# Performance work log

Measured on AMD Instinct MI355X. Metric: run time of the kernel, lower is better.

Reference implementation:

```python
import jax, jax.numpy as jnp
import numpy as np

B, T, N = 8, 512, 64        # batch, seq_len, enc_in
E, H, P = 128, 256, 96      # embed_size, hidden_size, pred_len
LAMBDA = 0.001              # softshrink sparsity threshold
SCALE = 0.02


def _leaky(h):
    return jnp.where(h >= 0, h, 0.01 * h)


def _softshrink(y):
    return jnp.where(y > LAMBDA, y - LAMBDA, jnp.where(y < -LAMBDA, y + LAMBDA, jnp.zeros_like(y)))


def setup_inputs() -> dict:
    key = jax.random.key(0)
    ks = jax.random.split(key, 16)
    f32 = jnp.float32
    d = {
        "x": jax.random.normal(ks[0], (B, T, N), f32),
        "emb": jax.random.normal(ks[1], (1, E), f32),
        # MLP (embed_size -> hidden -> embed_size), stored as [in, out]
        "w1": SCALE * jax.random.normal(ks[2], (E, H), f32),
        "b1": SCALE * jax.random.normal(ks[3], (H,), f32),
        "w2": SCALE * jax.random.normal(ks[4], (H, E), f32),
        "b2": SCALE * jax.random.normal(ks[5], (E,), f32),
        # MLP_time (seq_len -> hidden -> seq_len)
        "tw1": SCALE * jax.random.normal(ks[6], (T, H), f32),
        "tb1": SCALE * jax.random.normal(ks[7], (H,), f32),
        "tw2": SCALE * jax.random.normal(ks[8], (H, T), f32),
        "tb2": SCALE * jax.random.normal(ks[9], (T,), f32),
        # fc (seq_len*embed -> hidden -> pred_len)
        "fw1": SCALE * jax.random.normal(ks[10], (T * E, H), f32),
        "fb1": SCALE * jax.random.normal(ks[11], (H,), f32),
        "fw2": SCALE * jax.random.normal(ks[12], (H, P), f32),
        "fb2": SCALE * jax.random.normal(ks[13], (P,), f32),
    }
    return d


def reference(x, emb, w1, b1, w2, b2, tw1, tb1, tw2, tb2, fw1, fb1, fw2, fb2):
    # x: [B, T, N]
    x_noD = jnp.transpose(x, (0, 2, 1))            # [B, N, T]
    xe = x_noD[..., None] * emb                    # tokenEmb -> [B, N, T, E]
    bias = xe + x_noD[..., None]

    # NorMLP_temporal: rfft over time, shared MLP on real/imag, softshrink, irfft
    xf = jnp.fft.rfft(xe, axis=2, norm="ortho")   # [B, N, T//2+1, E] complex64

    def mlp(z):
        return _leaky(z @ w1 + b1) @ w2 + b2

    yr = _softshrink(mlp(xf.real))
    yi = _softshrink(mlp(xf.imag))
    y = jax.lax.complex(yr, yi)
    xt = jnp.fft.irfft(y, n=T, axis=2, norm="ortho")  # [B, N, T, E]

    # NorMLP_temporal_WO_freq: MLP_time over last (time) dim of x_noD
    xn = _leaky(x_noD @ tw1 + tb1) @ tw2 + tb2        # [B, N, T]

    out = xt + xn[..., None] + bias                   # use_bias = 1

    flat = out.reshape(B, N, T * E)
    h = _leaky(flat @ fw1 + fb1) @ fw2 + fb2          # [B, N, P]
    return jnp.transpose(h, (0, 2, 1))                # [B, P, N]
```

## Files before the change

kernel.cpp:

```cpp
#include <hip/hip_runtime.h>
#include <hip/hip_bf16.h>


typedef unsigned int uint;
typedef unsigned short ushort_t;
typedef __attribute__((ext_vector_type(4))) float f32x4;
typedef __attribute__((ext_vector_type(8))) short short8;

#define LAMBDA_ 0.001f
#define RSQRT512 0.044194173824159220f

__device__ __forceinline__ ushort_t f2bf(float f) {
    uint u = __float_as_uint(f);
    uint r = (u + 0x7FFFu + ((u >> 16) & 1u)) >> 16;
    return (ushort_t)r;
}
__device__ __forceinline__ ushort_t f2bf_hw(float f) {
    union { __hip_bfloat16 h; ushort_t u; } c;
    c.h = __float2bfloat16(f);
    return c.u;
}
__device__ __forceinline__ float bf2f(ushort_t v) { return __uint_as_float(((uint)v) << 16); }
__device__ __forceinline__ float leaky_(float v) { return v >= 0.f ? v : 0.01f * v; }

__device__ __forceinline__ void gload_lds16(const ushort_t* g, ushort_t* l) {
    __builtin_amdgcn_global_load_lds((const __attribute__((address_space(1))) void*)g,
                                     (__attribute__((address_space(3))) void*)l, 16, 0, 0);
}

__global__ __launch_bounds__(256) void k_pre(const float* __restrict__ x, const float* __restrict__ tw1,
                                             const float* __restrict__ tw2,
                                             ushort_t* __restrict__ A1cat, ushort_t* __restrict__ B1cat,
                                             ushort_t* __restrict__ Wt, ushort_t* __restrict__ tw2_bf) {
    __shared__ float tile[64 * 65];
    int bid = blockIdx.x;
    int tid = threadIdx.x;
    if (bid < 3072) {
        int region = bid >> 10;
        int id = ((bid & 1023) << 8) + tid;
        int a = id >> 9, c = id & 511;
        if (region == 0) {
            int f = (a <= 256) ? a : (a - 256);
            int m = (c * f) & 511;
            float ang = (float)m * (6.283185307179586f / 512.0f);
            float v = ((a <= 256) ? cosf(ang) : -sinf(ang)) * RSQRT512;
            ushort_t hi = f2bf(v);
            ushort_t lo = f2bf(v - bf2f(hi));
            size_t row = (size_t)a * 1536;
            B1cat[row + c] = hi;
            B1cat[row + 512 + c] = hi;
            B1cat[row + 1024 + c] = lo;
        } else if (region == 1) {
            int f = (a <= 256) ? a : (a - 256);
            int m = (c * f) & 511;
            float ang = (float)m * (6.283185307179586f / 512.0f);
            float v = ((a <= 256) ? cosf(ang) : -sinf(ang)) * RSQRT512;
            float sc = (a == 0 || a == 256) ? 1.0f : 2.0f;
            Wt[id] = f2bf(v * sc);
        } else {
            if ((bid & 1023) < 512) tw2_bf[id] = f2bf(tw2[id]);
        }
    } else if (bid < 3104) {
        int b = bid - 3072;
        int t0 = (b & 7) << 6, h0 = (b >> 3) << 6;
        float (*t64)[65] = (float(*)[65])tile;
        for (int i = 0; i < 16; ++i) {
            int idx = tid + i * 256;
            int r = idx >> 6, cc = idx & 63;
            t64[r][cc] = tw1[(size_t)(t0 + r) * 256 + h0 + cc];
        }
        __syncthreads();
        for (int i = 0; i < 16; ++i) {
            int idx = tid + i * 256;
            int rr = idx >> 6, cc2 = idx & 63;
            float v = t64[cc2][rr];
            ushort_t hi = f2bf(v);
            ushort_t lo = f2bf(v - bf2f(hi));
            size_t row = (size_t)(512 + h0 + rr) * 1536;
            int t = t0 + cc2;
            B1cat[row + t] = hi;
            B1cat[row + 512 + t] = hi;
            B1cat[row + 1024 + t] = lo;
        }
    } else {
        int b = bid - 3104;
        int bb = b >> 5;
        int rem = b & 31;
        int t0 = (rem >> 1) << 5;
        int n0 = (rem & 1) << 5;
        int tx = tid & 31, ty = tid >> 5;
        float (*t32)[33] = (float(*)[33])tile;
        for (int i = 0; i < 4; ++i) {
            int tt = ty * 4 + i;
            t32[tt][tx] = x[(size_t)(bb * 512 + t0 + tt) * 64 + n0 + tx];
        }
        __syncthreads();
        for (int i = 0; i < 4; ++i) {
            int nn = ty * 4 + i;
            float v = t32[tx][nn];
            ushort_t hi = f2bf(v);
            ushort_t lo = f2bf(v - bf2f(hi));
            size_t row = (size_t)(bb * 64 + n0 + nn) * 1536;
            int t = t0 + tx;
            A1cat[row + t] = hi;
            A1cat[row + 512 + t] = lo;
            A1cat[row + 1024 + t] = hi;
        }
    }
}

__global__ __launch_bounds__(256) void k_prep1(const float* __restrict__ emb, const float* __restrict__ w1,
                                               const float* __restrict__ b1,
                                               float* __restrict__ u_g, int* __restrict__ idxs_g,
                                               float* __restrict__ bpkey_g) {
    __shared__ float key_s[256];
    __shared__ int idx_s[256];
    int tid = threadIdx.x;
    float acc = 0.f;
#pragma unroll 8
    for (int e = 0; e < 128; ++e) acc += emb[e] * w1[e * 256 + tid];
    u_g[tid] = acc;
    float bb0 = b1[tid];
    key_s[tid] = (acc == 0.f) ? INFINITY : (-bb0 / acc);
    idx_s[tid] = tid;
    __syncthreads();
    for (int k = 2; k <= 256; k <<= 1) {
        for (int j = k >> 1; j > 0; j >>= 1) {
            int ixj = tid ^ j;
            if (ixj > tid) {
                bool up = ((tid & k) == 0);
                float a0 = key_s[tid], a1 = key_s[ixj];
                if ((a0 > a1) == up) {
                    key_s[tid] = a1; key_s[ixj] = a0;
                    int t0 = idx_s[tid]; idx_s[tid] = idx_s[ixj]; idx_s[ixj] = t0;
                }
            }
            __syncthreads();
        }
    }
    bpkey_g[tid] = key_s[tid];
    idxs_g[tid] = idx_s[tid];
}

__global__ __launch_bounds__(256) void k_prep2(const float* __restrict__ u_g, const float* __restrict__ b1,
                                               const float* __restrict__ w2, const float* __restrict__ b2,
                                               const int* __restrict__ idxs_g,
                                               ushort_t* __restrict__ Atab, ushort_t* __restrict__ Btab) {
    __shared__ float sA[256], sB[256];
    int e = blockIdx.x, r = threadIdx.x;
    float uu0 = u_g[r], bb0 = b1[r];
    float w0 = w2[r * 128 + e];
    float c = (uu0 < 0.f || (uu0 == 0.f && bb0 >= 0.f)) ? 1.0f : 0.01f;
    float bA = c * uu0 * w0, bB = c * bb0 * w0;
    int h = idxs_g[r];
    float uu = u_g[h], bb = b1[h];
    float w = w2[h * 128 + e];
    float sgn = (uu > 0.f) ? 0.99f : -0.99f;
    float dA = sgn * uu * w, dB = sgn * bb * w;
    sA[r] = bA; sB[r] = bB;
    __syncthreads();
    for (int off = 128; off > 0; off >>= 1) {
        if (r < off) { sA[r] += sA[r + off]; sB[r] += sB[r + off]; }
        __syncthreads();
    }
    float baseA = sA[0], baseB = sB[0] + b2[e];
    __syncthreads();
    sA[r] = dA; sB[r] = dB;
    __syncthreads();
    for (int off = 1; off < 256; off <<= 1) {
        float vA = (r >= off) ? sA[r - off] : 0.f;
        float vB = (r >= off) ? sB[r - off] : 0.f;
        __syncthreads();
        sA[r] += vA; sB[r] += vB;
        __syncthreads();
    }
    if (r == 0) { Atab[e] = f2bf(baseA); Btab[e] = f2bf(baseB); }
    Atab[(r + 1) * 128 + e] = f2bf(baseA + sA[r]);
    Btab[(r + 1) * 128 + e] = f2bf(baseB + sB[r]);
}

__global__ __launch_bounds__(256) void k_transpose_fw1(const float* __restrict__ fw1, ushort_t* __restrict__ fw1T) {
    __shared__ float tile[64][65];
    int bid = blockIdx.x;
    int e  = bid & 127;
    int hb = (bid >> 7) & 3;
    int tt = bid >> 9;
    int t0 = tt << 6, h0 = hb << 6;
    int tid = threadIdx.x;
    for (int i = 0; i < 4; ++i) {
        int idx = tid + i * 256;
        int r = idx >> 4, c4 = idx & 15;
        const float* src = fw1 + ((size_t)(t0 + r) * 128 + e) * 256 + h0 + c4 * 4;
        float4 v = *(const float4*)src;
        tile[r][c4 * 4 + 0] = v.x;
        tile[r][c4 * 4 + 1] = v.y;
        tile[r][c4 * 4 + 2] = v.z;
        tile[r][c4 * 4 + 3] = v.w;
    }
    __syncthreads();
    for (int p = 0; p < 2; ++p) {
        int idx = tid + p * 256;
        int hh = idx >> 3, tg = idx & 7;
        short8 o;
        for (int j = 0; j < 8; ++j) o[j] = (short)f2bf(tile[tg * 8 + j][hh]);
        *(short8*)(fw1T + ((size_t)(h0 + hh) * 128 + e) * 512 + t0 + tg * 8) = o;
    }
}

__global__ __launch_bounds__(256) void k_reduce_F2(const ushort_t* __restrict__ fw1T, const float* __restrict__ emb,
                                                   float* __restrict__ F1T) {
    __shared__ float embs[128];
    int h = blockIdx.x;
    int tid = threadIdx.x;
    if (tid < 128) embs[tid] = 1.f + emb[tid];
    __syncthreads();
    int t2 = tid * 2;
    const ushort_t* base = fw1T + ((size_t)h << 16) + t2;
    float as0 = 0.f, as1 = 0.f, ae0 = 0.f, ae1 = 0.f;
#pragma unroll 4
    for (int e = 0; e < 128; ++e) {
        uint v = *(const uint*)(base + (size_t)e * 512);
        float v0 = bf2f((ushort_t)(v & 0xffff));
        float v1 = bf2f((ushort_t)(v >> 16));
        float w = embs[e];
        as0 += v0; as1 += v1;
        ae0 += w * v0; ae1 += w * v1;
    }
    F1T[(size_t)h * 512 + t2] = as0;
    F1T[(size_t)h * 512 + t2 + 1] = as1;
    F1T[131072 + (size_t)h * 512 + t2] = ae0;
    F1T[131072 + (size_t)h * 512 + t2 + 1] = ae1;
}

__global__ __launch_bounds__(64) void k_pack_F(const float* __restrict__ F1sT, const float* __restrict__ F1eT,
                                               const float* __restrict__ tb2,
                                               ushort_t* __restrict__ B1cat, ushort_t* __restrict__ F1sT_bf,
                                               float* __restrict__ p2v) {
    int h = blockIdx.x;
    int lane = threadIdx.x;
    int t = lane * 8;
    float p2 = 0.f;
    short8 shi, ehi, elo;
    for (int j = 0; j < 8; ++j) {
        float vs = F1sT[(size_t)h * 512 + t + j];
        float ve = F1eT[(size_t)h * 512 + t + j];
        p2 += tb2[t + j] * vs;
        shi[j] = (short)f2bf(vs);
        ushort_t hi = f2bf(ve);
        ehi[j] = (short)hi;
        elo[j] = (short)f2bf(ve - bf2f(hi));
    }
    *(short8*)(F1sT_bf + (size_t)h * 512 + t) = shi;
    size_t row = (size_t)(768 + h) * 1536;
    *(short8*)(B1cat + row + t) = ehi;
    *(short8*)(B1cat + row + 512 + t) = ehi;
    *(short8*)(B1cat + row + 1024 + t) = elo;
    for (int o = 32; o > 0; o >>= 1) p2 += __shfl_xor(p2, o);
    if (lane == 0) p2v[h] = p2;
}

__global__ __launch_bounds__(256) void k_g1(const ushort_t* __restrict__ A, const ushort_t* __restrict__ Bm,
                                            float* __restrict__ partialG) {
    __shared__ ushort_t As[128 * 72];
    __shared__ ushort_t Bs[128 * 72];
    int tid = threadIdx.x;
    int lane = tid & 63, wid = tid >> 6;
    int wr = wid >> 1, wc = wid & 1;
    int bid = blockIdx.x;
    int kch = bid & 7, tilei = bid >> 3;
    int nt = tilei & 7, mt = tilei >> 3;
    int m0 = mt * 128, n0 = nt * 128;
    f32x4 acc[4][4] = {};
    for (int kt = 0; kt < 3; ++kt) {
        int kb = kch * 192 + kt * 64;
        __syncthreads();
        {
            uint4 va[4], vb[4];
            for (int i = 0; i < 4; ++i) {
                int q = tid + i * 256;
                int row = q >> 3, kcc = (q & 7) << 3;
                va[i] = *(const uint4*)(A + (size_t)(m0 + row) * 1536 + kb + kcc);
                vb[i] = *(const uint4*)(Bm + (size_t)(n0 + row) * 1536 + kb + kcc);
            }
            for (int i = 0; i < 4; ++i) {
                int q = tid + i * 256;
                int row = q >> 3, kcc = (q & 7) << 3;
                *(uint4*)&As[row * 72 + kcc] = va[i];
                *(uint4*)&Bs[row * 72 + kcc] = vb[i];
            }
        }
        __syncthreads();
        for (int ks = 0; ks < 2; ++ks) {
            short8 a[4], b[4];
            int kk = ks * 32 + (lane >> 4) * 8;
            for (int mi = 0; mi < 4; ++mi)
                a[mi] = *(const short8*)&As[(wr * 64 + mi * 16 + (lane & 15)) * 72 + kk];
            for (int ni = 0; ni < 4; ++ni)
                b[ni] = *(const short8*)&Bs[(wc * 64 + ni * 16 + (lane & 15)) * 72 + kk];
            for (int mi = 0; mi < 4; ++mi)
                for (int ni = 0; ni < 4; ++ni)
                    acc[mi][ni] = __builtin_amdgcn_mfma_f32_16x16x32_bf16(a[mi], b[ni], acc[mi][ni], 0, 0, 0);
        }
    }
    float* pbase = partialG + (size_t)kch * 524288;
    int mb0 = m0 + wr * 64 + ((lane >> 4) << 2);
    int nb0 = n0 + wc * 64 + (lane & 15);
    for (int mi = 0; mi < 4; ++mi)
        for (int ni = 0; ni < 4; ++ni) {
            int mbase = mb0 + mi * 16;
            int n = nb0 + ni * 16;
            for (int r = 0; r < 4; ++r)
                pbase[(size_t)(mbase + r) * 1024 + n] = acc[mi][ni][r];
        }
}

__global__ __launch_bounds__(256) void k_reduceG1(const float* __restrict__ partialG, const float* __restrict__ tb1,
                                                  float* __restrict__ s, ushort_t* __restrict__ hl,
                                                  float* __restrict__ h2c) {
    int id = blockIdx.x * 256 + threadIdx.x;
    int m = id >> 10, n = id & 1023;
    float acc = 0.f;
#pragma unroll
    for (int kc = 0; kc < 8; ++kc)
        acc += partialG[(size_t)kc * 524288 + id];
    if (n < 512) s[(size_t)m * 512 + n] = acc;
    else if (n < 768) hl[(size_t)m * 256 + (n - 512)] = f2bf(leaky_(acc + tb1[n - 512]));
    else h2c[(size_t)m * 256 + (n - 768)] = acc;
}

__global__ __launch_bounds__(256) void k_p2(const ushort_t* __restrict__ A, const ushort_t* __restrict__ Bm,
                                            ushort_t* __restrict__ P2T) {
    __shared__ ushort_t As[128 * 72];
    __shared__ ushort_t Bs[128 * 72];
    int tid = threadIdx.x;
    int lane = tid & 63, wid = tid >> 6;
    int wr = wid >> 1, wc = wid & 1;
    int bid = blockIdx.x;
    int nt = bid & 1, mt = bid >> 1;
    int m0 = mt * 128, n0 = nt * 128;
    f32x4 acc[4][4] = {};
    for (int kt = 0; kt < 8; ++kt) {
        int kb = kt * 64;
        __syncthreads();
        {
            uint4 va[4], vb[4];
            for (int i = 0; i < 4; ++i) {
                int q = tid + i * 256;
                int row = q >> 3, kcc = (q & 7) << 3;
                va[i] = *(const uint4*)(A + (size_t)(m0 + row) * 512 + kb + kcc);
                vb[i] = *(const uint4*)(Bm + (size_t)(n0 + row) * 512 + kb + kcc);
            }
            for (int i = 0; i < 4; ++i) {
                int q = tid + i * 256;
                int row = q >> 3, kcc = (q & 7) << 3;
                *(uint4*)&As[row * 72 + kcc] = va[i];
                *(uint4*)&Bs[row * 72 + kcc] = vb[i];
            }
        }
        __syncthreads();
        for (int ks = 0; ks < 2; ++ks) {
            short8 a[4], b[4];
            int kk = ks * 32 + (lane >> 4) * 8;
            for (int mi = 0; mi < 4; ++mi)
                a[mi] = *(const short8*)&As[(wr * 64 + mi * 16 + (lane & 15)) * 72 + kk];
            for (int ni = 0; ni < 4; ++ni)
                b[ni] = *(const short8*)&Bs[(wc * 64 + ni * 16 + (lane & 15)) * 72 + kk];
            for (int mi = 0; mi < 4; ++mi)
                for (int ni = 0; ni < 4; ++ni)
                    acc[mi][ni] = __builtin_amdgcn_mfma_f32_16x16x32_bf16(a[mi], b[ni], acc[mi][ni], 0, 0, 0);
        }
    }
    int mb0 = m0 + wr * 64 + ((lane >> 4) << 2);
    int nb0 = n0 + wc * 64 + (lane & 15);
    for (int mi = 0; mi < 4; ++mi)
        for (int ni = 0; ni < 4; ++ni) {
            int mbase = mb0 + mi * 16;
            int n = nb0 + ni * 16;
            ushort4 o;
            o.x = f2bf(acc[mi][ni][0]);
            o.y = f2bf(acc[mi][ni][1]);
            o.z = f2bf(acc[mi][ni][2]);
            o.w = f2bf(acc[mi][ni][3]);
            *(ushort4*)(P2T + (size_t)n * 256 + mbase) = o;
        }
}

__global__ __launch_bounds__(512) void k_gemm0(const ushort_t* __restrict__ A, const ushort_t* __restrict__ Bm,
                                               ushort_t* __restrict__ M2T) {
    __shared__ ushort_t As[2][128 * 64];
    __shared__ ushort_t Bs[2][128 * 64];
    int tid = threadIdx.x;
    int lane = tid & 63, wid = tid >> 6;
    int wr = wid >> 2, wc = wid & 3;
    int bid = blockIdx.x;
    int xx = bid & 7, y = bid >> 3;
    int mt = y & 3;
    int nt = ((y >> 2) << 3) | xx;
    int m0 = mt * 128, n0 = nt * 128;
    int lrow = lane >> 3;
    int sg = (lane & 7) ^ lrow;
    auto issue = [&](int kt, int buf) {
        int kb = kt * 64;
        for (int i = 0; i < 2; ++i) {
            int rbase = wid * 16 + i * 8;
            gload_lds16(A + (size_t)(m0 + rbase + lrow) * 512 + kb + sg * 8, &As[buf][wid * 1024 + i * 512]);
            gload_lds16(Bm + (size_t)(n0 + rbase + lrow) * 512 + kb + sg * 8, &Bs[buf][wid * 1024 + i * 512]);
        }
    };
    f32x4 acc[4][2] = {};
    issue(0, 0);
    __syncthreads();
    int cur = 0;
    for (int kt = 0; kt < 8; ++kt) {
        int nxt = cur ^ 1;
        if (kt + 1 < 8) issue(kt + 1, nxt);
        __builtin_amdgcn_s_setprio(1);
        for (int ks = 0; ks < 2; ++ks) {
            short8 a[4], b[2];
            int sl = ks * 4 + (lane >> 4);
            for (int mi = 0; mi < 4; ++mi) {
                int row = wr * 64 + mi * 16 + (lane & 15);
                a[mi] = *(const short8*)&As[cur][row * 64 + ((sl ^ (row & 7)) << 3)];
            }
            for (int ni = 0; ni < 2; ++ni) {
                int row = wc * 32 + ni * 16 + (lane & 15);
                b[ni] = *(const short8*)&Bs[cur][row * 64 + ((sl ^ (row & 7)) << 3)];
            }
            for (int mi = 0; mi < 4; ++mi)
                for (int ni = 0; ni < 2; ++ni)
                    acc[mi][ni] = __builtin_amdgcn_mfma_f32_16x16x32_bf16(a[mi], b[ni], acc[mi][ni], 0, 0, 0);
        }
        __builtin_amdgcn_s_setprio(0);
        __syncthreads();
        cur = nxt;
    }
    ushort_t* cstage = &As[0][0];
    for (int mi = 0; mi < 4; ++mi) {
        int ml = wr * 64 + mi * 16 + ((lane >> 4) << 2);
        for (int ni = 0; ni < 2; ++ni) {
            int nl = wc * 32 + ni * 16 + (lane & 15);
            for (int r = 0; r < 4; ++r) {
                int row = ml + r;
                cstage[row * 128 + (nl ^ ((row & 7) << 4))] = f2bf(acc[mi][ni][r]);
            }
        }
    }
    __syncthreads();
    short8* d8 = (short8*)(M2T + ((size_t)(n0 >> 7) << 16) + (size_t)m0 * 128);
    for (int i = 0; i < 4; ++i) {
        int p = tid + i * 512;
        int row = p >> 4;
        int col0 = (p & 15) * 8;
        d8[p] = *(const short8*)&cstage[row * 128 + (col0 ^ ((row & 7) << 4))];
    }
}

__global__ __launch_bounds__(512) void k_gemm1(const float* __restrict__ s,
                                               const ushort_t* __restrict__ Atab, const ushort_t* __restrict__ Btab,
                                               const float* __restrict__ bpkey,
                                               const ushort_t* __restrict__ Bm,
                                               float* __restrict__ partial) {
    __shared__ ushort_t As[2][128 * 64];
    __shared__ ushort_t Bs[2][256 * 64];
    __shared__ float sv_s[1024];
    __shared__ ushort_t r_s[1024];
    __shared__ float bp_s[256];
    int tid = threadIdx.x;
    int lane = tid & 63, wid = tid >> 6;
    int wr = wid >> 2, wc = wid & 3;
    int bid = blockIdx.x;
    int xcd = bid & 7, j = bid >> 3;
    int kcl = j & 7, mt = j >> 3;
    int kc = xcd * 8 + kcl;
    int m0 = mt * 128;
    int k0 = kc * 1024;
    if (tid < 256) bp_s[tid] = bpkey[tid];
    __syncthreads();
    {
        int row = tid >> 2, j2 = (tid & 3) * 2;
        float2 sv2 = *(const float2*)(s + (size_t)(m0 + row) * 512 + kc * 8 + j2);
        float svv[2] = {sv2.x, sv2.y};
        for (int q = 0; q < 2; ++q) {
            float sv = svv[q];
            int lo = 0, hi = 256;
            while (lo < hi) { int mid = (lo + hi) >> 1; if (bp_s[mid] <= sv) lo = mid + 1; else hi = mid; }
            sv_s[row * 8 + j2 + q] = sv;
            r_s[row * 8 + j2 + q] = (ushort_t)lo;
        }
    }
    __syncthreads();

    int lrow = lane >> 3;
    int sg = (lane & 7) ^ lrow;
    auto issueB = [&](int kt, int buf) {
        int kb = k0 + kt * 64;
        for (int i = 0; i < 4; ++i) {
            int rbase = wid * 32 + i * 8;
            gload_lds16(Bm + (size_t)(rbase + lrow) * 65536 + kb + sg * 8, &Bs[buf][wid * 2048 + i * 512]);
        }
    };
    short8 ta[2], tb[2];
    float svr[2];
    auto gather = [&](int kt) {
        int kl = kt >> 1;
        for (int i = 0; i < 2; ++i) {
            int q = tid + i * 512;
            int row = q >> 3, slot = q & 7;
            int e0 = ((kt & 1) << 6) + slot * 8;
            int r = r_s[row * 8 + kl];
            svr[i] = sv_s[row * 8 + kl];
            ta[i] = *(const short8*)(Atab + r * 128 + e0);
            tb[i] = *(const short8*)(Btab + r * 128 + e0);
        }
    };
    auto cookwrite = [&](int buf) {
        for (int i = 0; i < 2; ++i) {
            int q = tid + i * 512;
            int row = q >> 3, slot = q & 7;
            float sv = svr[i];
            short8 o;
            for (int jj = 0; jj < 8; ++jj) {
                float y = fmaf(sv, bf2f((ushort_t)ta[i][jj]), bf2f((ushort_t)tb[i][jj]));
                y = y - fminf(fmaxf(y, -LAMBDA_), LAMBDA_);
                o[jj] = (short)f2bf_hw(y);
            }
            *(short8*)&As[buf][row * 64 + ((slot ^ (row & 7)) << 3)] = o;
        }
    };

    f32x4 acc[4][4] = {};
    issueB(0, 0);
    gather(0);
    cookwrite(0);
    __syncthreads();
    int cur = 0;
    for (int kt = 0; kt < 16; ++kt) {
        int nxt = cur ^ 1;
        if (kt + 1 < 16) { issueB(kt + 1, nxt); gather(kt + 1); }
        __builtin_amdgcn_s_setprio(1);
        for (int ks = 0; ks < 2; ++ks) {
            short8 a[4], b[4];
            int sl = ks * 4 + (lane >> 4);
            for (int mi = 0; mi < 4; ++mi) {
                int row = wr * 64 + mi * 16 + (lane & 15);
                a[mi] = *(const short8*)&As[cur][row * 64 + ((sl ^ (row & 7)) << 3)];
            }
            for (int ni = 0; ni < 4; ++ni) {
                int row = wc * 64 + ni * 16 + (lane & 15);
                b[ni] = *(const short8*)&Bs[cur][row * 64 + ((sl ^ (row & 7)) << 3)];
            }
            for (int mi = 0; mi < 4; ++mi)
                for (int ni = 0; ni < 4; ++ni)
                    acc[mi][ni] = __builtin_amdgcn_mfma_f32_16x16x32_bf16(a[mi], b[ni], acc[mi][ni], 0, 0, 0);
        }
        __builtin_amdgcn_s_setprio(0);
        if (kt + 1 < 16) cookwrite(nxt);
        __syncthreads();
        cur = nxt;
    }
    int mb0 = m0 + wr * 64 + ((lane >> 4) << 2);
    int nb0 = wc * 64 + (lane & 15);
    float* pbase = partial + (size_t)kc * 131072;
    for (int mi = 0; mi < 4; ++mi)
        for (int ni = 0; ni < 4; ++ni) {
            int mbase = mb0 + mi * 16;
            int n = nb0 + ni * 16;
            for (int r = 0; r < 4; ++r)
                pbase[(size_t)(mbase + r) * 256 + n] = acc[mi][ni][r];
        }
}

__global__ __launch_bounds__(128) void k_final(const float* __restrict__ partial, const ushort_t* __restrict__ hl,
                                               const ushort_t* __restrict__ P2T, const float* __restrict__ p2v,
                                               const float* __restrict__ h2c, const float* __restrict__ fb1,
                                               const float* __restrict__ fw2, const float* __restrict__ fb2,
                                               float* __restrict__ out) {
    __shared__ float a_s[256];
    __shared__ float hl_s[256];
    int bn = blockIdx.x;
    int tid = threadIdx.x;
    {
        uint v = *(const uint*)(hl + (size_t)bn * 256 + tid * 2);
        hl_s[tid * 2] = bf2f((ushort_t)(v & 0xffff));
        hl_s[tid * 2 + 1] = bf2f((ushort_t)(v >> 16));
    }
    __syncthreads();
    for (int p = 0; p < 2; ++p) {
        int i = tid + p * 128;
        float acc = p2v[i] + h2c[(size_t)bn * 256 + i] + fb1[i];
#pragma unroll 8
        for (int kc = 0; kc < 64; ++kc)
            acc += partial[((size_t)kc * 512 + bn) * 256 + i];
        const ushort_t* prow = P2T + (size_t)i * 256;
#pragma unroll 4
        for (int jb = 0; jb < 32; ++jb) {
            short8 pv = *(const short8*)(prow + jb * 8);
            for (int j8 = 0; j8 < 8; ++j8)
                acc += hl_s[jb * 8 + j8] * bf2f((ushort_t)pv[j8]);
        }
        a_s[i] = leaky_(acc);
    }
    __syncthreads();
    if (tid < 96) {
        float acc = fb2[tid];
        for (int hh = 0; hh < 256; ++hh)
            acc += a_s[hh] * fw2[hh * 96 + tid];
        int b = bn >> 6, n = bn & 63;
        out[(size_t)(b * 96 + tid) * 64 + n] = acc;
    }
}

extern "C" void kernel_launch(void* const* d_in, const int* in_sizes, int n_in,
                              void* d_out, int out_size, void* d_ws, size_t ws_size,
                              hipStream_t stream) {
    const float* x   = (const float*)d_in[0];
    const float* emb = (const float*)d_in[1];
    const float* w1  = (const float*)d_in[2];
    const float* b1  = (const float*)d_in[3];
    const float* w2  = (const float*)d_in[4];
    const float* b2  = (const float*)d_in[5];
    const float* tw1 = (const float*)d_in[6];
    const float* tb1 = (const float*)d_in[7];
    const float* tw2 = (const float*)d_in[8];
    const float* tb2 = (const float*)d_in[9];
    const float* fw1 = (const float*)d_in[10];
    const float* fb1 = (const float*)d_in[11];
    const float* fw2 = (const float*)d_in[12];
    const float* fb2 = (const float*)d_in[13];
    float* out = (float*)d_out;

    char* W = (char*)d_ws;
    size_t off = 0;
    auto take = [&](size_t bytes) { size_t r = off; off += (bytes + 255) & ~(size_t)255; return r; };
    ushort_t* fw1T  = (ushort_t*)(W + take(33554432));
    ushort_t* M2T   = (ushort_t*)(W + take(33554432));
    float* partial  = (float*)(W + take(64 * 512 * 256 * 4));
    float* partialG = (float*)(W + take(8 * 512 * 1024 * 4));
    ushort_t* A1cat = (ushort_t*)(W + take(512 * 1536 * 2));
    ushort_t* B1cat = (ushort_t*)(W + take(1024 * 1536 * 2));
    ushort_t* Wt    = (ushort_t*)(W + take(512 * 512 * 2));
    ushort_t* tw2bf = (ushort_t*)(W + take(256 * 512 * 2));
    float* F1T      = (float*)(W + take(2 * 256 * 512 * 4));
    ushort_t* F1sbf = (ushort_t*)(W + take(256 * 512 * 2));
    float* sbuf     = (float*)(W + take(512 * 512 * 4));
    ushort_t* hlbuf = (ushort_t*)(W + take(512 * 256 * 2));
    float* h2c      = (float*)(W + take(512 * 256 * 4));
    ushort_t* P2T   = (ushort_t*)(W + take(256 * 256 * 2));
    float* p2v      = (float*)(W + take(256 * 4));
    ushort_t* Atab  = (ushort_t*)(W + take(257 * 128 * 2));
    ushort_t* Btab  = (ushort_t*)(W + take(257 * 128 * 2));
    float* bpkey    = (float*)(W + take(256 * 4));
    float* u_g      = (float*)(W + take(256 * 4));
    int* idxs_g     = (int*)(W + take(256 * 4));
    (void)ws_size; (void)in_sizes; (void)n_in; (void)out_size;

    k_pre<<<3360, 256, 0, stream>>>(x, tw1, tw2, A1cat, B1cat, Wt, tw2bf);
    k_prep1<<<1, 256, 0, stream>>>(emb, w1, b1, u_g, idxs_g, bpkey);
    k_prep2<<<128, 256, 0, stream>>>(u_g, b1, w2, b2, idxs_g, Atab, Btab);
    k_transpose_fw1<<<4096, 256, 0, stream>>>(fw1, fw1T);
    k_reduce_F2<<<256, 256, 0, stream>>>(fw1T, emb, F1T);
    k_pack_F<<<256, 64, 0, stream>>>(F1T, F1T + 131072, tb2, B1cat, F1sbf, p2v);
    k_g1<<<256, 256, 0, stream>>>(A1cat, B1cat, partialG);
    k_reduceG1<<<2048, 256, 0, stream>>>(partialG, tb1, sbuf, hlbuf, h2c);
    k_gemm0<<<1024, 512, 0, stream>>>(Wt, fw1T, M2T);
    k_p2<<<4, 256, 0, stream>>>(tw2bf, F1sbf, P2T);
    k_gemm1<<<256, 512, 0, stream>>>(sbuf, Atab, Btab, bpkey, M2T, partial);
    k_final<<<512, 128, 0, stream>>>(partial, hlbuf, P2T, p2v, h2c, fb1, fw2, fb2, out);
}
```

Measured before the change: 165.3 us.

## Merge independent prep and GEMM kernels into fewer multi-role launches

Folds the twelve launches into six by giving each fused kernel block-index ranges for independent jobs: pre-pack, fw1 transpose and the breakpoint sort share one launch, the F reduction/pack and the table build share another, the g1 and p2 GEMMs share one, and the partialG reduction rides along with gemm0. k_reduce_F2 and k_pack_F are combined so the fp32 F1T intermediate is dropped and bf16 outputs are written directly, with p2v now reduced through LDS. The aim is to cut launch gaps and let small kernels overlap with larger ones. The cost is larger LDS and register footprints from the role union, which can lower occupancy, plus a single-block bitonic sort and a tiny p2 job that may finish late and extend their fused launches.

```diff
diff --git a/kernel.cpp b/kernel.cpp
--- a/kernel.cpp
+++ b/kernel.cpp
@@ -28,11 +28,18 @@
                                      (__attribute__((address_space(3))) void*)l, 16, 0, 0);
 }
 
-__global__ __launch_bounds__(256) void k_pre(const float* __restrict__ x, const float* __restrict__ tw1,
-                                             const float* __restrict__ tw2,
-                                             ushort_t* __restrict__ A1cat, ushort_t* __restrict__ B1cat,
-                                             ushort_t* __restrict__ Wt, ushort_t* __restrict__ tw2_bf) {
+__global__ __launch_bounds__(256) void k_pre_plus(const float* __restrict__ x, const float* __restrict__ tw1,
+                                                  const float* __restrict__ tw2, const float* __restrict__ fw1,
+                                                  const float* __restrict__ emb, const float* __restrict__ w1,
+                                                  const float* __restrict__ b1,
+                                                  ushort_t* __restrict__ A1cat, ushort_t* __restrict__ B1cat,
+                                                  ushort_t* __restrict__ Wt, ushort_t* __restrict__ tw2_bf,
+                                                  ushort_t* __restrict__ fw1T,
+                                                  float* __restrict__ u_g, int* __restrict__ idxs_g,
+                                                  float* __restrict__ bpkey_g) {
     __shared__ float tile[64 * 65];
+    __shared__ float key_s[256];
+    __shared__ int idx_s[256];
     int bid = blockIdx.x;
     int tid = threadIdx.x;
     if (bid < 3072) {
@@ -82,7 +89,7 @@
             B1cat[row + 512 + t] = hi;
             B1cat[row + 1024 + t] = lo;
         }
-    } else {
+    } else if (bid < 3360) {
         int b = bid - 3104;
         int bb = b >> 5;
         int rem = b & 31;
@@ -106,293 +113,267 @@
             A1cat[row + 512 + t] = lo;
             A1cat[row + 1024 + t] = hi;
         }
-    }
-}
-
-__global__ __launch_bounds__(256) void k_prep1(const float* __restrict__ emb, const float* __restrict__ w1,
-                                               const float* __restrict__ b1,
-                                               float* __restrict__ u_g, int* __restrict__ idxs_g,
-                                               float* __restrict__ bpkey_g) {
-    __shared__ float key_s[256];
-    __shared__ int idx_s[256];
+    } else if (bid < 7456) {
+        int b = bid - 3360;
+        int e  = b & 127;
+        int hb = (b >> 7) & 3;
+        int tt = b >> 9;
+        int t0 = tt << 6, h0 = hb << 6;
+        float (*t64)[65] = (float(*)[65])tile;
+        for (int i = 0; i < 4; ++i) {
+            int idx = tid + i * 256;
+            int r = idx >> 4, c4 = idx & 15;
+            const float* src = fw1 + ((size_t)(t0 + r) * 128 + e) * 256 + h0 + c4 * 4;
+            float4 v = *(const float4*)src;
+            t64[r][c4 * 4 + 0] = v.x;
+            t64[r][c4 * 4 + 1] = v.y;
+            t64[r][c4 * 4 + 2] = v.z;
+            t64[r][c4 * 4 + 3] = v.w;
+        }
+        __syncthreads();
+        for (int p = 0; p < 2; ++p) {
+            int idx = tid + p * 256;
+            int hh = idx >> 3, tg = idx & 7;
+            short8 o;
+            for (int j = 0; j < 8; ++j) o[j] = (short)f2bf(t64[tg * 8 + j][hh]);
+            *(short8*)(fw1T + ((size_t)(h0 + hh) * 128 + e) * 512 + t0 + tg * 8) = o;
+        }
+    } else {
+        float acc = 0.f;
+#pragma unroll 8
+        for (int e = 0; e < 128; ++e) acc += emb[e] * w1[e * 256 + tid];
+        u_g[tid] = acc;
+        float bb0 = b1[tid];
+        key_s[tid] = (acc == 0.f) ? INFINITY : (-bb0 / acc);
+        idx_s[tid] = tid;
+        __syncthreads();
+        for (int k = 2; k <= 256; k <<= 1) {
+            for (int j = k >> 1; j > 0; j >>= 1) {
+                int ixj = tid ^ j;
+                if (ixj > tid) {
+                    bool up = ((tid & k) == 0);
+                    float a0 = key_s[tid], a1 = key_s[ixj];
+                    if ((a0 > a1) == up) {
+                        key_s[tid] = a1; key_s[ixj] = a0;
+                        int t0 = idx_s[tid]; idx_s[tid] = idx_s[ixj]; idx_s[ixj] = t0;
+                    }
+                }
+                __syncthreads();
+            }
+        }
+        bpkey_g[tid] = key_s[tid];
+        idxs_g[tid] = idx_s[tid];
+    }
+}
+
+__global__ __launch_bounds__(256) void k_mid(const ushort_t* __restrict__ fw1T, const float* __restrict__ emb,
+                                             const float* __restrict__ tb2,
+                                             ushort_t* __restrict__ B1cat, ushort_t* __restrict__ F1sbf,
+                                             float* __restrict__ p2v,
+                                             const float* __restrict__ u_g, const float* __restrict__ b1,
+                                             const float* __restrict__ w2, const float* __restrict__ b2,
+                                             const int* __restrict__ idxs_g,
+                                             ushort_t* __restrict__ Atab, ushort_t* __restrict__ Btab) {
+    __shared__ float embs[128];
+    __shared__ float red[256];
+    __shared__ float sA[256], sB[256];
+    int bid = blockIdx.x;
     int tid = threadIdx.x;
-    float acc = 0.f;
-#pragma unroll 8
-    for (int e = 0; e < 128; ++e) acc += emb[e] * w1[e * 256 + tid];
-    u_g[tid] = acc;
-    float bb0 = b1[tid];
-    key_s[tid] = (acc == 0.f) ? INFINITY : (-bb0 / acc);
-    idx_s[tid] = tid;
-    __syncthreads();
-    for (int k = 2; k <= 256; k <<= 1) {
-        for (int j = k >> 1; j > 0; j >>= 1) {
-            int ixj = tid ^ j;
-            if (ixj > tid) {
-                bool up = ((tid & k) == 0);
-                float a0 = key_s[tid], a1 = key_s[ixj];
-                if ((a0 > a1) == up) {
-                    key_s[tid] = a1; key_s[ixj] = a0;
-                    int t0 = idx_s[tid]; idx_s[tid] = idx_s[ixj]; idx_s[ixj] = t0;
-                }
-            }
-            __syncthreads();
-        }
-    }
-    bpkey_g[tid] = key_s[tid];
-    idxs_g[tid] = idx_s[tid];
-}
-
-__global__ __launch_bounds__(256) void k_prep2(const float* __restrict__ u_g, const float* __restrict__ b1,
-                                               const float* __restrict__ w2, const float* __restrict__ b2,
-                                               const int* __restrict__ idxs_g,
-                                               ushort_t* __restrict__ Atab, ushort_t* __restrict__ Btab) {
-    __shared__ float sA[256], sB[256];
-    int e = blockIdx.x, r = threadIdx.x;
-    float uu0 = u_g[r], bb0 = b1[r];
-    float w0 = w2[r * 128 + e];
-    float c = (uu0 < 0.f || (uu0 == 0.f && bb0 >= 0.f)) ? 1.0f : 0.01f;
-    float bA = c * uu0 * w0, bB = c * bb0 * w0;
-    int h = idxs_g[r];
-    float uu = u_g[h], bb = b1[h];
-    float w = w2[h * 128 + e];
-    float sgn = (uu > 0.f) ? 0.99f : -0.99f;
-    float dA = sgn * uu * w, dB = sgn * bb * w;
-    sA[r] = bA; sB[r] = bB;
-    __syncthreads();
-    for (int off = 128; off > 0; off >>= 1) {
-        if (r < off) { sA[r] += sA[r + off]; sB[r] += sB[r + off]; }
-        __syncthreads();
-    }
-    float baseA = sA[0], baseB = sB[0] + b2[e];
-    __syncthreads();
-    sA[r] = dA; sB[r] = dB;
-    __syncthreads();
-    for (int off = 1; off < 256; off <<= 1) {
-        float vA = (r >= off) ? sA[r - off] : 0.f;
-        float vB = (r >= off) ? sB[r - off] : 0.f;
-        __syncthreads();
-        sA[r] += vA; sB[r] += vB;
-        __syncthreads();
-    }
-    if (r == 0) { Atab[e] = f2bf(baseA); Btab[e] = f2bf(baseB); }
-    Atab[(r + 1) * 128 + e] = f2bf(baseA + sA[r]);
-    Btab[(r + 1) * 128 + e] = f2bf(baseB + sB[r]);
-}
-
-__global__ __launch_bounds__(256) void k_transpose_fw1(const float* __restrict__ fw1, ushort_t* __restrict__ fw1T) {
-    __shared__ float tile[64][65];
-    int bid = blockIdx.x;
-    int e  = bid & 127;
-    int hb = (bid >> 7) & 3;
-    int tt = bid >> 9;
-    int t0 = tt << 6, h0 = hb << 6;
-    int tid = threadIdx.x;
-    for (int i = 0; i < 4; ++i) {
-        int idx = tid + i * 256;
-        int r = idx >> 4, c4 = idx & 15;
-        const float* src = fw1 + ((size_t)(t0 + r) * 128 + e) * 256 + h0 + c4 * 4;
-        float4 v = *(const float4*)src;
-        tile[r][c4 * 4 + 0] = v.x;
-        tile[r][c4 * 4 + 1] = v.y;
-        tile[r][c4 * 4 + 2] = v.z;
-        tile[r][c4 * 4 + 3] = v.w;
-    }
-    __syncthreads();
-    for (int p = 0; p < 2; ++p) {
-        int idx = tid + p * 256;
-        int hh = idx >> 3, tg = idx & 7;
-        short8 o;
-        for (int j = 0; j < 8; ++j) o[j] = (short)f2bf(tile[tg * 8 + j][hh]);
-        *(short8*)(fw1T + ((size_t)(h0 + hh) * 128 + e) * 512 + t0 + tg * 8) = o;
-    }
-}
-
-__global__ __launch_bounds__(256) void k_reduce_F2(const ushort_t* __restrict__ fw1T, const float* __restrict__ emb,
-                                                   float* __restrict__ F1T) {
-    __shared__ float embs[128];
-    int h = blockIdx.x;
-    int tid = threadIdx.x;
-    if (tid < 128) embs[tid] = 1.f + emb[tid];
-    __syncthreads();
-    int t2 = tid * 2;
-    const ushort_t* base = fw1T + ((size_t)h << 16) + t2;
-    float as0 = 0.f, as1 = 0.f, ae0 = 0.f, ae1 = 0.f;
+    if (bid < 256) {
+        int h = bid;
+        if (tid < 128) embs[tid] = 1.f + emb[tid];
+        __syncthreads();
+        int t2 = tid * 2;
+        const ushort_t* base = fw1T + ((size_t)h << 16) + t2;
+        float as0 = 0.f, as1 = 0.f, ae0 = 0.f, ae1 = 0.f;
 #pragma unroll 4
-    for (int e = 0; e < 128; ++e) {
-        uint v = *(const uint*)(base + (size_t)e * 512);
-        float v0 = bf2f((ushort_t)(v & 0xffff));
-        float v1 = bf2f((ushort_t)(v >> 16));
-        float w = embs[e];
-        as0 += v0; as1 += v1;
-        ae0 += w * v0; ae1 += w * v1;
-    }
-    F1T[(size_t)h * 512 + t2] = as0;
-    F1T[(size_t)h * 512 + t2 + 1] = as1;
-    F1T[131072 + (size_t)h * 512 + t2] = ae0;
-    F1T[131072 + (size_t)h * 512 + t2 + 1] = ae1;
-}
-
-__global__ __launch_bounds__(64) void k_pack_F(const float* __restrict__ F1sT, const float* __restrict__ F1eT,
-                                               const float* __restrict__ tb2,
-                                               ushort_t* __restrict__ B1cat, ushort_t* __restrict__ F1sT_bf,
-                                               float* __restrict__ p2v) {
-    int h = blockIdx.x;
-    int lane = threadIdx.x;
-    int t = lane * 8;
-    float p2 = 0.f;
-    short8 shi, ehi, elo;
-    for (int j = 0; j < 8; ++j) {
-        float vs = F1sT[(size_t)h * 512 + t + j];
-        float ve = F1eT[(size_t)h * 512 + t + j];
-        p2 += tb2[t + j] * vs;
-        shi[j] = (short)f2bf(vs);
-        ushort_t hi = f2bf(ve);
-        ehi[j] = (short)hi;
-        elo[j] = (short)f2bf(ve - bf2f(hi));
-    }
-    *(short8*)(F1sT_bf + (size_t)h * 512 + t) = shi;
-    size_t row = (size_t)(768 + h) * 1536;
-    *(short8*)(B1cat + row + t) = ehi;
-    *(short8*)(B1cat + row + 512 + t) = ehi;
-    *(short8*)(B1cat + row + 1024 + t) = elo;
-    for (int o = 32; o > 0; o >>= 1) p2 += __shfl_xor(p2, o);
-    if (lane == 0) p2v[h] = p2;
-}
-
-__global__ __launch_bounds__(256) void k_g1(const ushort_t* __restrict__ A, const ushort_t* __restrict__ Bm,
-                                            float* __restrict__ partialG) {
+        for (int e = 0; e < 128; ++e) {
+            uint v = *(const uint*)(base + (size_t)e * 512);
+            float v0 = bf2f((ushort_t)(v & 0xffff));
+            float v1 = bf2f((ushort_t)(v >> 16));
+            float w = embs[e];
+            as0 += v0; as1 += v1;
+            ae0 += w * v0; ae1 += w * v1;
+        }
+        *(uint*)(F1sbf + (size_t)h * 512 + t2) = (uint)f2bf(as0) | ((uint)f2bf(as1) << 16);
+        ushort_t hi0 = f2bf(ae0), hi1 = f2bf(ae1);
+        ushort_t lo0 = f2bf(ae0 - bf2f(hi0)), lo1 = f2bf(ae1 - bf2f(hi1));
+        size_t row = (size_t)(768 + h) * 1536;
+        uint hpk = (uint)hi0 | ((uint)hi1 << 16);
+        *(uint*)(B1cat + row + t2) = hpk;
+        *(uint*)(B1cat + row + 512 + t2) = hpk;
+        *(uint*)(B1cat + row + 1024 + t2) = (uint)lo0 | ((uint)lo1 << 16);
+        red[tid] = tb2[t2] * as0 + tb2[t2 + 1] * as1;
+        __syncthreads();
+        for (int off = 128; off > 0; off >>= 1) {
+            if (tid < off) red[tid] += red[tid + off];
+            __syncthreads();
+        }
+        if (tid == 0) p2v[h] = red[0];
+    } else {
+        int e = bid - 256, r = tid;
+        float uu0 = u_g[r], bb0 = b1[r];
+        float w0 = w2[r * 128 + e];
+        float c = (uu0 < 0.f || (uu0 == 0.f && bb0 >= 0.f)) ? 1.0f : 0.01f;
+        float bA = c * uu0 * w0, bB = c * bb0 * w0;
+        int h = idxs_g[r];
+        float uu = u_g[h], bb = b1[h];
+        float w = w2[h * 128 + e];
+        float sgn = (uu > 0.f) ? 0.99f : -0.99f;
+        float dA = sgn * uu * w, dB = sgn * bb * w;
+        sA[r] = bA; sB[r] = bB;
+        __syncthreads();
+        for (int off = 128; off > 0; off >>= 1) {
+            if (r < off) { sA[r] += sA[r + off]; sB[r] += sB[r + off]; }
+            __syncthreads();
+        }
+        float baseA = sA[0], baseB = sB[0] + b2[e];
+        __syncthreads();
+        sA[r] = dA; sB[r] = dB;
+        __syncthreads();
+        for (int off = 1; off < 256; off <<= 1) {
+            float vA = (r >= off) ? sA[r - off] : 0.f;
+            float vB = (r >= off) ? sB[r - off] : 0.f;
+            __syncthreads();
+            sA[r] += vA; sB[r] += vB;
+            __syncthreads();
+        }
+        if (r == 0) { Atab[e] = f2bf(baseA); Btab[e] = f2bf(baseB); }
+        Atab[(r + 1) * 128 + e] = f2bf(baseA + sA[r]);
+        Btab[(r + 1) * 128 + e] = f2bf(baseB + sB[r]);
+    }
+}
+
+__global__ __launch_bounds__(256) void k_g1p2(const ushort_t* __restrict__ A, const ushort_t* __restrict__ Bm,
+                                              float* __restrict__ partialG,
+                                              const ushort_t* __restrict__ tw2bf, const ushort_t* __restrict__ F1sbf,
+                                              ushort_t* __restrict__ P2T) {
     __shared__ ushort_t As[128 * 72];
     __shared__ ushort_t Bs[128 * 72];
     int tid = threadIdx.x;
     int lane = tid & 63, wid = tid >> 6;
     int wr = wid >> 1, wc = wid & 1;
     int bid = blockIdx.x;
-    int kch = bid & 7, tilei = bid >> 3;
-    int nt = tilei & 7, mt = tilei >> 3;
-    int m0 = mt * 128, n0 = nt * 128;
     f32x4 acc[4][4] = {};
-    for (int kt = 0; kt < 3; ++kt) {
-        int kb = kch * 192 + kt * 64;
-        __syncthreads();
-        {
-            uint4 va[4], vb[4];
-            for (int i = 0; i < 4; ++i) {
-                int q = tid + i * 256;
-                int row = q >> 3, kcc = (q & 7) << 3;
-                va[i] = *(const uint4*)(A + (size_t)(m0 + row) * 1536 + kb + kcc);
-                vb[i] = *(const uint4*)(Bm + (size_t)(n0 + row) * 1536 + kb + kcc);
-            }
-            for (int i = 0; i < 4; ++i) {
-                int q = tid + i * 256;
-                int row = q >> 3, kcc = (q & 7) << 3;
-                *(uint4*)&As[row * 72 + kcc] = va[i];
-                *(uint4*)&Bs[row * 72 + kcc] = vb[i];
-            }
-        }
-        __syncthreads();
-        for (int ks = 0; ks < 2; ++ks) {
-            short8 a[4], b[4];
-            int kk = ks * 32 + (lane >> 4) * 8;
-            for (int mi = 0; mi < 4; ++mi)
-                a[mi] = *(const short8*)&As[(wr * 64 + mi * 16 + (lane & 15)) * 72 + kk];
-            for (int ni = 0; ni < 4; ++ni)
-                b[ni] = *(const short8*)&Bs[(wc * 64 + ni * 16 + (lane & 15)) * 72 + kk];
-            for (int mi = 0; mi < 4; ++mi)
+    if (bid < 256) {
+        int kch = bid & 7, tilei = bid >> 3;
+        int nt = tilei & 7, mt = tilei >> 3;
+        int m0 = mt * 128, n0 = nt * 128;
+        for (int kt = 0; kt < 3; ++kt) {
+            int kb = kch * 192 + kt * 64;
+            __syncthreads();
+            {
+                uint4 va[4], vb[4];
+                for (int i = 0; i < 4; ++i) {
+                    int q = tid + i * 256;
+                    int row = q >> 3, kcc = (q & 7) << 3;
+                    va[i] = *(const uint4*)(A + (size_t)(m0 + row) * 1536 + kb + kcc);
+                    vb[i] = *(const uint4*)(Bm + (size_t)(n0 + row) * 1536 + kb + kcc);
+                }
+                for (int i = 0; i < 4; ++i) {
+                    int q = tid + i * 256;
+                    int row = q >> 3, kcc = (q & 7) << 3;
+                    *(uint4*)&As[row * 72 + kcc] = va[i];
+                    *(uint4*)&Bs[row * 72 + kcc] = vb[i];
+                }
+            }
+            __syncthreads();
+            for (int ks = 0; ks < 2; ++ks) {
+                short8 a[4], b[4];
+                int kk = ks * 32 + (lane >> 4) * 8;
+                for (int mi = 0; mi < 4; ++mi)
+                    a[mi] = *(const short8*)&As[(wr * 64 + mi * 16 + (lane & 15)) * 72 + kk];
                 for (int ni = 0; ni < 4; ++ni)
-                    acc[mi][ni] = __builtin_amdgcn_mfma_f32_16x16x32_bf16(a[mi], b[ni], acc[mi][ni], 0, 0, 0);
-        }
-    }
-    float* pbase = partialG + (size_t)kch * 524288;
-    int mb0 = m0 + wr * 64 + ((lane >> 4) << 2);
-    int nb0 = n0 + wc * 64 + (lane & 15);
-    for (int mi = 0; mi < 4; ++mi)
-        for (int ni = 0; ni < 4; ++ni) {
-            int mbase = mb0 + mi * 16;
-            int n = nb0 + ni * 16;
-            for (int r = 0; r < 4; ++r)
-                pbase[(size_t)(mbase + r) * 1024 + n] = acc[mi][ni][r];
-        }
-}
-
-__global__ __launch_bounds__(256) void k_reduceG1(const float* __restrict__ partialG, const float* __restrict__ tb1,
-                                                  float* __restrict__ s, ushort_t* __restrict__ hl,
-                                                  float* __restrict__ h2c) {
-    int id = blockIdx.x * 256 + threadIdx.x;
-    int m = id >> 10, n = id & 1023;
-    float acc = 0.f;
-#pragma unroll
-    for (int kc = 0; kc < 8; ++kc)
-        acc += partialG[(size_t)kc * 524288 + id];
-    if (n < 512) s[(size_t)m * 512 + n] = acc;
-    else if (n < 768) hl[(size_t)m * 256 + (n - 512)] = f2bf(leaky_(acc + tb1[n - 512]));
-    else h2c[(size_t)m * 256 + (n - 768)] = acc;
-}
-
-__global__ __launch_bounds__(256) void k_p2(const ushort_t* __restrict__ A, const ushort_t* __restrict__ Bm,
-                                            ushort_t* __restrict__ P2T) {
-    __shared__ ushort_t As[128 * 72];
-    __shared__ ushort_t Bs[128 * 72];
-    int tid = threadIdx.x;
-    int lane = tid & 63, wid = tid >> 6;
-    int wr = wid >> 1, wc = wid & 1;
-    int bid = blockIdx.x;
-    int nt = bid & 1, mt = bid >> 1;
-    int m0 = mt * 128, n0 = nt * 128;
-    f32x4 acc[4][4] = {};
-    for (int kt = 0; kt < 8; ++kt) {
-        int kb = kt * 64;
-        __syncthreads();
-        {
-            uint4 va[4], vb[4];
-            for (int i = 0; i < 4; ++i) {
-                int q = tid + i * 256;
-                int row = q >> 3, kcc = (q & 7) << 3;
-                va[i] = *(const uint4*)(A + (size_t)(m0 + row) * 512 + kb + kcc);
-                vb[i] = *(const uint4*)(Bm + (size_t)(n0 + row) * 512 + kb + kcc);
-            }
-            for (int i = 0; i < 4; ++i) {
-                int q = tid + i * 256;
-                int row = q >> 3, kcc = (q & 7) << 3;
-                *(uint4*)&As[row * 72 + kcc] = va[i];
-                *(uint4*)&Bs[row * 72 + kcc] = vb[i];
-            }
-        }
-        __syncthreads();
-        for (int ks = 0; ks < 2; ++ks) {
-            short8 a[4], b[4];
-            int kk = ks * 32 + (lane >> 4) * 8;
-            for (int mi = 0; mi < 4; ++mi)
-                a[mi] = *(const short8*)&As[(wr * 64 + mi * 16 + (lane & 15)) * 72 + kk];
-            for (int ni = 0; ni < 4; ++ni)
-                b[ni] = *(const short8*)&Bs[(wc * 64 + ni * 16 + (lane & 15)) * 72 + kk];
-            for (int mi = 0; mi < 4; ++mi)
+                    b[ni] = *(const short8*)&Bs[(wc * 64 + ni * 16 + (lane & 15)) * 72 + kk];
+                for (int mi = 0; mi < 4; ++mi)
+                    for (int ni = 0; ni < 4; ++ni)
+                        acc[mi][ni] = __builtin_amdgcn_mfma_f32_16x16x32_bf16(a[mi], b[ni], acc[mi][ni], 0, 0, 0);
+            }
+        }
+        float* pbase = partialG + (size_t)kch * 524288;
+        int mb0 = m0 + wr * 64 + ((lane >> 4) << 2);
+        int nb0 = n0 + wc * 64 + (lane & 15);
+        for (int mi = 0; mi < 4; ++mi)
+            for (int ni = 0; ni < 4; ++ni) {
+                int mbase = mb0 + mi * 16;
+                int n = nb0 + ni * 16;
+                for (int r = 0; r < 4; ++r)
+                    pbase[(size_t)(mbase + r) * 1024 + n] = acc[mi][ni][r];
+            }
+    } else {
+        int b2i = bid - 256;
+        int nt = b2i & 1, mt = b2i >> 1;
+        int m0 = mt * 128, n0 = nt * 128;
+        for (int kt = 0; kt < 8; ++kt) {
+            int kb = kt * 64;
+            __syncthreads();
+            {
+                uint4 va[4], vb[4];
+                for (int i = 0; i < 4; ++i) {
+                    int q = tid + i * 256;
+                    int row = q >> 3, kcc = (q & 7) << 3;
+                    va[i] = *(const uint4*)(tw2bf + (size_t)(m0 + row) * 512 + kb + kcc);
+                    vb[i] = *(const uint4*)(F1sbf + (size_t)(n0 + row) * 512 + kb + kcc);
+                }
+                for (int i = 0; i < 4; ++i) {
+                    int q = tid + i * 256;
+                    int row = q >> 3, kcc = (q & 7) << 3;
+                    *(uint4*)&As[row * 72 + kcc] = va[i];
+                    *(uint4*)&Bs[row * 72 + kcc] = vb[i];
+                }
+            }
+            __syncthreads();
+            for (int ks = 0; ks < 2; ++ks) {
+                short8 a[4], b[4];
+                int kk = ks * 32 + (lane >> 4) * 8;
+                for (int mi = 0; mi < 4; ++mi)
+                    a[mi] = *(const short8*)&As[(wr * 64 + mi * 16 + (lane & 15)) * 72 + kk];
                 for (int ni = 0; ni < 4; ++ni)
-                    acc[mi][ni] = __builtin_amdgcn_mfma_f32_16x16x32_bf16(a[mi], b[ni], acc[mi][ni], 0, 0, 0);
-        }
-    }
-    int mb0 = m0 + wr * 64 + ((lane >> 4) << 2);
-    int nb0 = n0 + wc * 64 + (lane & 15);
-    for (int mi = 0; mi < 4; ++mi)
-        for (int ni = 0; ni < 4; ++ni) {
-            int mbase = mb0 + mi * 16;
-            int n = nb0 + ni * 16;
-            ushort4 o;
-            o.x = f2bf(acc[mi][ni][0]);
-            o.y = f2bf(acc[mi][ni][1]);
-            o.z = f2bf(acc[mi][ni][2]);
-            o.w = f2bf(acc[mi][ni][3]);
-            *(ushort4*)(P2T + (size_t)n * 256 + mbase) = o;
-        }
-}
-
-__global__ __launch_bounds__(512) void k_gemm0(const ushort_t* __restrict__ A, const ushort_t* __restrict__ Bm,
-                                               ushort_t* __restrict__ M2T) {
+                    b[ni] = *(const short8*)&Bs[(wc * 64 + ni * 16 + (lane & 15)) * 72 + kk];
+                for (int mi = 0; mi < 4; ++mi)
+                    for (int ni = 0; ni < 4; ++ni)
+                        acc[mi][ni] = __builtin_amdgcn_mfma_f32_16x16x32_bf16(a[mi], b[ni], acc[mi][ni], 0, 0, 0);
+            }
+        }
+        int mb0 = m0 + wr * 64 + ((lane >> 4) << 2);
+        int nb0 = n0 + wc * 64 + (lane & 15);
+        for (int mi = 0; mi < 4; ++mi)
+            for (int ni = 0; ni < 4; ++ni) {
+                int mbase = mb0 + mi * 16;
+                int n = nb0 + ni * 16;
+                ushort4 o;
+                o.x = f2bf(acc[mi][ni][0]);
+                o.y = f2bf(acc[mi][ni][1]);
+                o.z = f2bf(acc[mi][ni][2]);
+                o.w = f2bf(acc[mi][ni][3]);
+                *(ushort4*)(P2T + (size_t)n * 256 + mbase) = o;
+            }
+    }
+}
+
+__global__ __launch_bounds__(512) void k_gemm0r(const ushort_t* __restrict__ A, const ushort_t* __restrict__ Bm,
+                                                ushort_t* __restrict__ M2T,
+                                                const float* __restrict__ partialG, const float* __restrict__ tb1,
+                                                float* __restrict__ s, ushort_t* __restrict__ hl,
+                                                float* __restrict__ h2c) {
     __shared__ ushort_t As[2][128 * 64];
     __shared__ ushort_t Bs[2][128 * 64];
     int tid = threadIdx.x;
+    int bid = blockIdx.x;
+    if (bid >= 1024) {
+        int id = (bid - 1024) * 512 + tid;
+        int m = id >> 10, n = id & 1023;
+        float acc = 0.f;
+#pragma unroll
+        for (int kc = 0; kc < 8; ++kc)
+            acc += partialG[(size_t)kc * 524288 + id];
+        if (n < 512) s[(size_t)m * 512 + n] = acc;
+        else if (n < 768) hl[(size_t)m * 256 + (n - 512)] = f2bf(leaky_(acc + tb1[n - 512]));
+        else h2c[(size_t)m * 256 + (n - 768)] = acc;
+        return;
+    }
     int lane = tid & 63, wid = tid >> 6;
     int wr = wid >> 2, wc = wid & 3;
-    int bid = blockIdx.x;
     int xx = bid & 7, y = bid >> 3;
     int mt = y & 3;
     int nt = ((y >> 2) << 3) | xx;
@@ -640,7 +621,6 @@
     ushort_t* B1cat = (ushort_t*)(W + take(1024 * 1536 * 2));
     ushort_t* Wt    = (ushort_t*)(W + take(512 * 512 * 2));
     ushort_t* tw2bf = (ushort_t*)(W + take(256 * 512 * 2));
-    float* F1T      = (float*)(W + take(2 * 256 * 512 * 4));
     ushort_t* F1sbf = (ushort_t*)(W + take(256 * 512 * 2));
     float* sbuf     = (float*)(W + take(512 * 512 * 4));
     ushort_t* hlbuf = (ushort_t*)(W + take(512 * 256 * 2));
@@ -654,16 +634,12 @@
     int* idxs_g     = (int*)(W + take(256 * 4));
     (void)ws_size; (void)in_sizes; (void)n_in; (void)out_size;
 
-    k_pre<<<3360, 256, 0, stream>>>(x, tw1, tw2, A1cat, B1cat, Wt, tw2bf);
-    k_prep1<<<1, 256, 0, stream>>>(emb, w1, b1, u_g, idxs_g, bpkey);
-    k_prep2<<<128, 256, 0, stream>>>(u_g, b1, w2, b2, idxs_g, Atab, Btab);
-    k_transpose_fw1<<<4096, 256, 0, stream>>>(fw1, fw1T);
-    k_reduce_F2<<<256, 256, 0, stream>>>(fw1T, emb, F1T);
-    k_pack_F<<<256, 64, 0, stream>>>(F1T, F1T + 131072, tb2, B1cat, F1sbf, p2v);
-    k_g1<<<256, 256, 0, stream>>>(A1cat, B1cat, partialG);
-    k_reduceG1<<<2048, 256, 0, stream>>>(partialG, tb1, sbuf, hlbuf, h2c);
-    k_gemm0<<<1024, 512, 0, stream>>>(Wt, fw1T, M2T);
-    k_p2<<<4, 256, 0, stream>>>(tw2bf, F1sbf, P2T);
+    k_pre_plus<<<7457, 256, 0, stream>>>(x, tw1, tw2, fw1, emb, w1, b1,
+                                         A1cat, B1cat, Wt, tw2bf, fw1T, u_g, idxs_g, bpkey);
+    k_mid<<<384, 256, 0, stream>>>(fw1T, emb, tb2, B1cat, F1sbf, p2v,
+                                   u_g, b1, w2, b2, idxs_g, Atab, Btab);
+    k_g1p2<<<260, 256, 0, stream>>>(A1cat, B1cat, partialG, tw2bf, F1sbf, P2T);
+    k_gemm0r<<<2048, 512, 0, stream>>>(Wt, fw1T, M2T, partialG, tb1, sbuf, hlbuf, h2c);
     k_gemm1<<<256, 512, 0, stream>>>(sbuf, Atab, Btab, bpkey, M2T, partial);
     k_final<<<512, 128, 0, stream>>>(partial, hlbuf, P2T, p2v, h2c, fb1, fw2, fb2, out);
 }
```

New measurement: 141.3 us. 14.5% less time.
